# Kernel tuning notes

Measured on AMD Instinct MI355X. Metric: run time of the kernel, lower is better.

The kernel has to match this reference:

```python
import jax, jax.numpy as jnp
import numpy as np

N_NODES = 50000
N_EDGES = 800000
IN_CH = 128
HID = 48
HEADS = 2
HH = HID * HEADS  # 96
N_GRAPHS = 64
NEG_SLOPE = 0.2


def _gat_layer(x, src, dst, n, W, a_src, a_dst, b, heads, out_ch):
    # x: [N, in]; W: [in, heads*out]; a_src/a_dst: [heads, out]; b: [heads*out]
    h = (x @ W).reshape(n, heads, out_ch)              # [N, H, C]
    es = (h * a_src).sum(-1)                            # [N, H]
    ed = (h * a_dst).sum(-1)                            # [N, H]
    e = jax.nn.leaky_relu(es[src] + ed[dst], NEG_SLOPE)  # [E, H]
    m = jax.ops.segment_max(e, dst, num_segments=n)      # segment softmax (stable)
    p = jnp.exp(e - m[dst])
    denom = jax.ops.segment_sum(p, dst, num_segments=n)
    alpha = p / denom[dst]                               # [E, H]
    out = jax.ops.segment_sum(alpha[:, :, None] * h[src], dst, num_segments=n)
    return out.reshape(n, heads * out_ch) + b


def setup_inputs() -> dict:
    key = jax.random.key(0)
    ks = jax.random.split(key, 20)
    x = jax.random.normal(ks[0], (N_NODES, IN_CH), dtype=jnp.float32)
    edge_index = jax.random.randint(ks[1], (2, N_EDGES), 0, N_NODES, dtype=jnp.int64)
    edge_weight = jax.random.uniform(ks[2], (N_EDGES,), dtype=jnp.float32)
    batch = jnp.sort(jax.random.randint(ks[3], (N_NODES,), 0, N_GRAPHS, dtype=jnp.int64))
    s = 0.1
    params = {
        'W1': jax.random.normal(ks[4], (IN_CH, HH)) * s,
        'as1': jax.random.normal(ks[5], (HEADS, HID)) * s,
        'ad1': jax.random.normal(ks[6], (HEADS, HID)) * s,
        'b1': jnp.zeros((HH,), jnp.float32),
        'W2': jax.random.normal(ks[7], (HH, HH)) * s,
        'as2': jax.random.normal(ks[8], (1, HH)) * s,
        'ad2': jax.random.normal(ks[9], (1, HH)) * s,
        'b2': jnp.zeros((HH,), jnp.float32),
        'W3': jax.random.normal(ks[10], (HH, HH)) * s,
        'as3': jax.random.normal(ks[11], (1, HH)) * s,
        'ad3': jax.random.normal(ks[12], (1, HH)) * s,
        'b3': jnp.zeros((HH,), jnp.float32),
        'W4': jax.random.normal(ks[13], (HH, HH)) * s,
        'as4': jax.random.normal(ks[14], (1, HH)) * s,
        'ad4': jax.random.normal(ks[15], (1, HH)) * s,
        'b4': jnp.zeros((HH,), jnp.float32),
        'Wc': jax.random.normal(ks[16], (HH, 1)) * s,
        'bc': jnp.zeros((1,), jnp.float32),
    }
    return {'x': x, 'edge_index': edge_index, 'edge_weight': edge_weight,
            'batch': batch, **params}


def reference(x, edge_index, edge_weight, batch,
              W1, as1, ad1, b1, W2, as2, ad2, b2,
              W3, as3, ad3, b3, W4, as4, ad4, b4, Wc, bc):
    n = x.shape[0]
    loops = jnp.arange(n, dtype=edge_index.dtype)  # PyG GATConv add_self_loops=True
    src = jnp.concatenate([edge_index[0], loops])
    dst = jnp.concatenate([edge_index[1], loops])
    # edge_weight is ignored by GATConv when edge_dim=None (faithful to PyG)
    h = jax.nn.relu(_gat_layer(x, src, dst, n, W1, as1, ad1, b1, HEADS, HID))
    h = jax.nn.relu(_gat_layer(h, src, dst, n, W2, as2, ad2, b2, 1, HH))
    h = jax.nn.relu(_gat_layer(h, src, dst, n, W3, as3, ad3, b3, 1, HH))
    h = jax.nn.relu(_gat_layer(h, src, dst, n, W4, as4, ad4, b4, 1, HH))
    # global_mean_pool
    sums = jax.ops.segment_sum(h, batch, num_segments=N_GRAPHS)
    cnts = jax.ops.segment_sum(jnp.ones((n, 1), h.dtype), batch, num_segments=N_GRAPHS)
    pooled = sums / jnp.maximum(cnts, 1.0)
    return jax.nn.sigmoid(pooled @ Wc + bc)
```

## Files before the change

kernel.cpp:

```cpp
#include <hip/hip_runtime.h>
#include <hip/hip_bf16.h>

#define NN 50000
#define NE 800000
#define NG 64
#define NBUCK 256
#define BN 196
#define EPB 4096
#define HB 196
#define SMAX 4200

typedef __attribute__((ext_vector_type(8))) short short8;
typedef __attribute__((ext_vector_type(4))) float float4v;
typedef __attribute__((ext_vector_type(2))) float float2v;

__device__ __forceinline__ float bf2f(unsigned short u){
    unsigned v = ((unsigned)u) << 16; float f; __builtin_memcpy(&f, &v, 4); return f;
}
__device__ __forceinline__ unsigned short f2bf(float f){
    unsigned u; __builtin_memcpy(&u, &f, 4);
    u = (u + 0x7fffu + ((u >> 16) & 1u)) >> 16;
    return (unsigned short)u;
}
__device__ __forceinline__ float lrelu(float v){ return v > 0.f ? v : 0.2f * v; }

__device__ __forceinline__ float ldflex(const void* p, long i, int isbf){
    if (isbf) return bf2f(((const unsigned short*)p)[i]);
    return ((const float*)p)[i];
}
__device__ __forceinline__ int ldidx(const int* p, long i, int is64){
    return p[is64 ? (i << 1) : i];
}

__device__ __forceinline__ unsigned int enc_fp8_1(float f){
    unsigned u; __builtin_memcpy(&u, &f, 4);
    unsigned s = (u >> 24) & 0x80u;
    float a = fabsf(f); a = fminf(a, 448.f);
    float x = a * 0x1p-120f;
    unsigned xu; __builtin_memcpy(&xu, &x, 4);
    unsigned r = (xu + 0x7FFFFu + ((xu >> 20) & 1u)) >> 20;
    if (r > 0x7Eu) r = 0x7Eu;
    return s | r;
}
__device__ __forceinline__ unsigned short pk_fp8(float a, float b){
#if __has_builtin(__builtin_amdgcn_cvt_pk_fp8_f32)
    int r = __builtin_amdgcn_cvt_pk_fp8_f32(a, b, 0, false);
    return (unsigned short)(r & 0xFFFF);
#else
    return (unsigned short)(enc_fp8_1(a) | (enc_fp8_1(b) << 8));
#endif
}
__device__ __forceinline__ float dec_fp8_manual(unsigned int byte){
    unsigned bits = ((byte & 0x80u) << 24) | ((byte & 0x7Fu) << 20);
    float f; __builtin_memcpy(&f, &bits, 4);
    return f * 0x1p120f;
}
__device__ __forceinline__ void dec_fp8x4_pk(unsigned int v, float2v& lo, float2v& hi){
#if __has_builtin(__builtin_amdgcn_cvt_pk_f32_fp8)
    lo = __builtin_amdgcn_cvt_pk_f32_fp8((int)v, false);
    hi = __builtin_amdgcn_cvt_pk_f32_fp8((int)v, true);
#else
    lo[0] = dec_fp8_manual(v & 0xFF);
    lo[1] = dec_fp8_manual((v >> 8) & 0xFF);
    hi[0] = dec_fp8_manual((v >> 16) & 0xFF);
    hi[1] = dec_fp8_manual((v >> 24) & 0xFF);
#endif
}

__device__ __forceinline__ float rdlane_f(float v, int l){
    int i; __builtin_memcpy(&i, &v, 4);
    int r = __builtin_amdgcn_readlane(i, l);
    float f; __builtin_memcpy(&f, &r, 4);
    return f;
}

__global__ void detect_kernel(const unsigned short* xu, const unsigned int* eiu,
                              const unsigned int* bu, int* flags){
    if (threadIdx.x != 0 || blockIdx.x != 0) return;
    int hit = 0;
    for (int i = 0; i < 128; i++){
        int ex = (xu[2 * i] >> 7) & 0xFF;
        if (ex >= 100 && ex <= 140) hit++;
    }
    flags[0] = (hit >= 64) ? 1 : 0;
    int z = 0;
    for (int i = 0; i < 128; i++) if (eiu[2 * i + 1] == 0) z++;
    flags[1] = (z >= 120) ? 1 : 0;
    z = 0;
    for (int i = 0; i < 128; i++) if (bu[49745 + 2 * i] == 0) z++;
    flags[2] = (z >= 120) ? 1 : 0;
}

__global__ __launch_bounds__(256) void wtprep_kernel(const void* W0, const void* W1,
                                                     const void* W2, const void* W3,
                                                     unsigned short* wt_all,
                                                     const int* flags){
    int l = blockIdx.x;
    const void* W = (l == 0) ? W0 : (l == 1) ? W1 : (l == 2) ? W2 : W3;
    int K = (l == 0) ? 128 : 96;
    unsigned short* out = wt_all + ((l == 0) ? 0 : (96 * 128 + (l - 1) * 96 * 96));
    int isbf = flags[0];
    int tot = 96 * K;
    for (int i = threadIdx.x; i < tot; i += 256){
        int c = i / K, k = i - c * K;
        out[i] = f2bf(ldflex(W, (long)k * 96 + c, isbf));
    }
}

__global__ __launch_bounds__(256) void xconv_kernel(const void* x, unsigned short* xb,
                                                    const int* flags){
    int isbf = flags[0];
    long i8 = ((long)blockIdx.x * 256 + threadIdx.x) * 8;
    if (i8 >= (long)NN * 128) return;
    unsigned int o[4];
    #pragma unroll
    for (int j = 0; j < 4; j++){
        unsigned short a = f2bf(ldflex(x, i8 + 2 * j, isbf));
        unsigned short b = f2bf(ldflex(x, i8 + 2 * j + 1, isbf));
        o[j] = (unsigned)a | ((unsigned)b << 16);
    }
    *(uint4*)(xb + i8) = make_uint4(o[0], o[1], o[2], o[3]);
}

__global__ __launch_bounds__(256) void bhist_kernel(const int* __restrict__ ei,
                                                    int* __restrict__ bcnt,
                                                    const int* __restrict__ flags){
    __shared__ int h[NBUCK];
    int tid = threadIdx.x;
    h[tid] = 0; __syncthreads();
    int f64 = flags[1];
    long e0 = (long)blockIdx.x * EPB + tid;
    #pragma unroll
    for (int r = 0; r < 16; r++){
        long e = e0 + r * 256;
        if (e < NE){
            int d = ldidx(ei, NE + e, f64);
            atomicAdd(&h[d / BN], 1);
        }
    }
    __syncthreads();
    atomicAdd(&bcnt[tid], h[tid]);
}

__global__ __launch_bounds__(256) void bscan_kernel(const int* __restrict__ bcnt,
                                                    int* __restrict__ bbase,
                                                    int* __restrict__ bcur){
    __shared__ int sd[NBUCK];
    int tid = threadIdx.x;
    int v = bcnt[tid];
    sd[tid] = v; __syncthreads();
    for (int off = 1; off < 256; off <<= 1){
        int x = sd[tid];
        int y = (tid >= off) ? sd[tid - off] : 0;
        __syncthreads();
        sd[tid] = x + y;
        __syncthreads();
    }
    int excl = sd[tid] - v;
    bbase[tid] = excl;
    bcur[tid] = excl;
    if (tid == 255) bbase[256] = excl + v;
}

__global__ __launch_bounds__(256) void bscatter_kernel(const int* __restrict__ ei,
                                                       int* __restrict__ bcur,
                                                       int2* __restrict__ ebuf,
                                                       const int* __restrict__ flags){
    __shared__ int h[NBUCK], lofs[NBUCK], gbase[NBUCK], lcur[NBUCK];
    __shared__ int2 lstage[EPB];
    int tid = threadIdx.x;
    int f64 = flags[1];
    h[tid] = 0; __syncthreads();
    int2 ed[16]; int bk[16];
    long e0 = (long)blockIdx.x * EPB + tid;
    #pragma unroll
    for (int r = 0; r < 16; r++){
        long e = e0 + r * 256;
        if (e < NE){
            int s = ldidx(ei, e, f64);
            int d = ldidx(ei, NE + e, f64);
            ed[r] = make_int2(s, d);
            bk[r] = d / BN;
            atomicAdd(&h[bk[r]], 1);
        } else bk[r] = -1;
    }
    __syncthreads();
    int v = h[tid];
    lofs[tid] = v; __syncthreads();
    for (int off = 1; off < 256; off <<= 1){
        int x = lofs[tid];
        int y = (tid >= off) ? lofs[tid - off] : 0;
        __syncthreads();
        lofs[tid] = x + y;
        __syncthreads();
    }
    int excl = lofs[tid] - v;
    lofs[tid] = excl;
    lcur[tid] = excl;
    if (v > 0) gbase[tid] = atomicAdd(&bcur[tid], v);
    __syncthreads();
    #pragma unroll
    for (int r = 0; r < 16; r++){
        if (bk[r] >= 0){
            int p = atomicAdd(&lcur[bk[r]], 1);
            lstage[p] = ed[r];
        }
    }
    __syncthreads();
    long base = (long)blockIdx.x * EPB;
    int cnt = (NE - base < EPB) ? (int)(NE - base) : EPB;
    for (int j = tid; j < cnt; j += 256){
        int2 e = lstage[j];
        int i = e.y / BN;
        ebuf[gbase[i] + j - lofs[i]] = e;
    }
}

__global__ __launch_bounds__(256) void place_kernel(const int2* __restrict__ ebuf,
                                                    const int* __restrict__ bbase,
                                                    int* __restrict__ row_ptr,
                                                    int2* __restrict__ csr2){
    __shared__ int nh[BN];
    __shared__ int nofs[256];
    __shared__ int lcur[BN];
    __shared__ int2 stage[SMAX];
    int k = blockIdx.x, tid = threadIdx.x;
    int n0 = k * BN;
    int seg0 = bbase[k], len = bbase[k + 1] - seg0;
    for (int i = tid; i < BN; i += 256) nh[i] = 0;
    __syncthreads();
    for (int j = tid; j < len; j += 256){
        int2 e = ebuf[seg0 + j];
        atomicAdd(&nh[e.y - n0], 1);
    }
    __syncthreads();
    int v = (tid < BN) ? nh[tid] : 0;
    nofs[tid] = v; __syncthreads();
    for (int off = 1; off < 256; off <<= 1){
        int x = nofs[tid];
        int y = (tid >= off) ? nofs[tid - off] : 0;
        __syncthreads();
        nofs[tid] = x + y;
        __syncthreads();
    }
    int excl = nofs[tid] - v;
    if (tid < BN){
        lcur[tid] = excl;
        int node = n0 + tid;
        if (node < NN) row_ptr[node] = seg0 + excl;
    }
    if (k == NBUCK - 1 && tid == 0) row_ptr[NN] = NE;
    __syncthreads();
    if (len <= SMAX){
        for (int j = tid; j < len; j += 256){
            int2 e = ebuf[seg0 + j];
            int p = atomicAdd(&lcur[e.y - n0], 1);
            stage[p] = e;
        }
        __syncthreads();
        for (int j = tid; j < len; j += 256)
            csr2[seg0 + j] = stage[j];
    } else {
        for (int j = tid; j < len; j += 256){
            int2 e = ebuf[seg0 + j];
            int p = atomicAdd(&lcur[e.y - n0], 1);
            csr2[seg0 + p] = e;
        }
    }
}

template<int K, int H>
__global__ __launch_bounds__(256) void gemm_mfma(const unsigned short* __restrict__ A,
                                                 const unsigned short* __restrict__ Wt,
                                                 const void* __restrict__ as_,
                                                 const void* __restrict__ ad_,
                                                 unsigned short* __restrict__ hq16,
                                                 float* __restrict__ es,
                                                 float* __restrict__ ed,
                                                 float* __restrict__ pself,
                                                 const int* __restrict__ flags){
    __shared__ union {
        struct { unsigned short xs[64 * 40]; unsigned short wt[96 * 40]; } s;
        float hs[64 * 104];
    } u;
    int tid = threadIdx.x;
    int row0 = blockIdx.x * 64;
    int lane = tid & 63, w = tid >> 6;
    int m = lane & 15, q = lane >> 4;
    float4v acc[6];
    #pragma unroll
    for (int ct = 0; ct < 6; ct++) acc[ct] = (float4v){0.f, 0.f, 0.f, 0.f};

    int sr = tid >> 2, kp = tid & 3;
    int rr = row0 + sr; if (rr >= NN) rr = NN - 1;

    for (int k0 = 0; k0 < K; k0 += 32){
        *(uint4*)(u.s.xs + sr * 40 + kp * 8) =
            *(const uint4*)(A + (size_t)rr * K + k0 + kp * 8);
        for (int i = tid; i < 96 * 4; i += 256){
            int c = i >> 2, kq = i & 3;
            *(uint4*)(u.s.wt + c * 40 + kq * 8) =
                *(const uint4*)(Wt + (size_t)c * K + k0 + kq * 8);
        }
        __syncthreads();
        short8 a = *(const short8*)(u.s.xs + (w * 16 + m) * 40 + q * 8);
        #pragma unroll
        for (int ct = 0; ct < 6; ct++){
            short8 b = *(const short8*)(u.s.wt + (ct * 16 + m) * 40 + q * 8);
            acc[ct] = __builtin_amdgcn_mfma_f32_16x16x32_bf16(a, b, acc[ct], 0, 0, 0);
        }
        __syncthreads();
    }

    #pragma unroll
    for (int ct = 0; ct < 6; ct++)
        #pragma unroll
        for (int r = 0; r < 4; r++)
            u.hs[(w * 16 + q * 4 + r) * 104 + ct * 16 + m] = acc[ct][r];
    __syncthreads();

    int rl = tid >> 2, part = tid & 3;
    int row = row0 + rl;
    int isbf = flags[0];
    float hv[24];
    #pragma unroll
    for (int jj = 0; jj < 6; jj++)
        *(float4v*)&hv[jj * 4] = *(const float4v*)&u.hs[rl * 104 + part * 24 + jj * 4];

    float pes = 0.f, ped = 0.f;
    #pragma unroll
    for (int i = 0; i < 24; i++){
        int c = part * 24 + i;
        pes += hv[i] * ldflex(as_, c, isbf);
        ped += hv[i] * ldflex(ad_, c, isbf);
    }
    pes += __shfl_xor(pes, 1); ped += __shfl_xor(ped, 1);
    if (H == 1){ pes += __shfl_xor(pes, 2); ped += __shfl_xor(ped, 2); }

    if (row < NN){
        if (part == 0){
            es[(long)row * H] = pes; ed[(long)row * H] = ped;
            pself[(long)row * H] = __expf(lrelu(pes + ped));
        }
        if (H == 2 && part == 2){
            es[(long)row * H + 1] = pes; ed[(long)row * H + 1] = ped;
            pself[(long)row * H + 1] = __expf(lrelu(pes + ped));
        }
        unsigned short wds[12];
        #pragma unroll
        for (int j = 0; j < 12; j++) wds[j] = pk_fp8(hv[2 * j], hv[2 * j + 1]);
        uint2* dst = (uint2*)hq16 + (long)row * 16 + part * 3;
        #pragma unroll
        for (int j2 = 0; j2 < 3; j2++){
            uint2 v;
            v.x = (unsigned)wds[4 * j2] | ((unsigned)wds[4 * j2 + 1] << 16);
            v.y = (unsigned)wds[4 * j2 + 2] | ((unsigned)wds[4 * j2 + 3] << 16);
            dst[j2] = v;
        }
    }
}

template<int H>
__global__ __launch_bounds__(256) void pexp_kernel(const float* __restrict__ es,
                                                   const float* __restrict__ ed,
                                                   const int2* __restrict__ csr2,
                                                   void* __restrict__ edata){
    int i = blockIdx.x * 256 + threadIdx.x;
    if (i >= NE) return;
    int2 e = csr2[i];
    if (H == 1){
        float p = __expf(lrelu(es[e.x] + ed[e.y]));
        ((uint2*)edata)[i] = make_uint2((unsigned)e.x, __float_as_uint(p));
    } else {
        float p0 = __expf(lrelu(es[2 * (long)e.x] + ed[2 * (long)e.y]));
        float p1 = __expf(lrelu(es[2 * (long)e.x + 1] + ed[2 * (long)e.y + 1]));
        ((uint4*)edata)[i] = make_uint4((unsigned)e.x, __float_as_uint(p0),
                                        __float_as_uint(p1), 0u);
    }
}

template<int H>
__global__ __launch_bounds__(256) void attn_kernel(const unsigned int* __restrict__ hq,
                                                   const void* __restrict__ edata,
                                                   const float* __restrict__ pself,
                                                   const int* __restrict__ row_ptr,
                                                   const void* __restrict__ bias,
                                                   unsigned int* __restrict__ outb,
                                                   const int* __restrict__ flags){
    int lane = threadIdx.x & 63;
    int d = blockIdx.x * 4 + (threadIdx.x >> 6);
    if (d >= NN) return;
    int isbf = flags[0];
    int beg = row_ptr[d], deg = row_ptr[d + 1] - beg;
    int g = (lane >= 24 && lane < 48) ? 1 : 0;
    int c = lane - g * 24;
    bool head0 = (c < 12);
    int m = lane - 48;

    int s_nxt = 0; float p0_nxt = 0.f, p1_nxt = 0.f;
    if (lane >= 48 && m < deg){
        if (H == 1){
            uint2 e = ((const uint2*)edata)[beg + m];
            s_nxt = (int)e.x; p0_nxt = __uint_as_float(e.y);
        } else {
            uint4 e = ((const uint4*)edata)[beg + m];
            s_nxt = (int)e.x; p0_nxt = __uint_as_float(e.y); p1_nxt = __uint_as_float(e.z);
        }
    }

    float2v acc01 = {0.f, 0.f}, acc23 = {0.f, 0.f};
    float dn0 = 0.f, dn1 = 0.f;
    for (int base = 0; base < deg; base += 16){
        int s_cur = s_nxt; float p0c = p0_nxt, p1c = p1_nxt;
        dn0 += p0c; dn1 += p1c;
        int nb = base + 16;
        s_nxt = 0; p0_nxt = 0.f; p1_nxt = 0.f;
        if (lane >= 48 && nb + m < deg){
            if (H == 1){
                uint2 e = ((const uint2*)edata)[beg + nb + m];
                s_nxt = (int)e.x; p0_nxt = __uint_as_float(e.y);
            } else {
                uint4 e = ((const uint4*)edata)[beg + nb + m];
                s_nxt = (int)e.x; p0_nxt = __uint_as_float(e.y); p1_nxt = __uint_as_float(e.z);
            }
        }
        unsigned int v[8]; float pv[8];
        #pragma unroll
        for (int jj = 0; jj < 8; jj++){
            int idx = 48 + 2 * jj + g;
            int s = __shfl(s_cur, idx);
            float p0 = __shfl(p0c, idx);
            float p;
            if (H == 2){
                float p1 = __shfl(p1c, idx);
                p = head0 ? p0 : p1;
            } else p = p0;
            pv[jj] = p;
            v[jj] = (lane < 48) ? hq[(unsigned)s * 32u + (unsigned)c] : 0u;
        }
        #pragma unroll
        for (int jj = 0; jj < 8; jj++){
            float2v lo, hi;
            dec_fp8x4_pk(v[jj], lo, hi);
            float2v p2 = {pv[jj], pv[jj]};
            acc01 += p2 * lo;
            acc23 += p2 * hi;
        }
    }

    for (int off = 1; off < 16; off <<= 1){
        dn0 += __shfl_xor(dn0, off);
        if (H == 2) dn1 += __shfl_xor(dn1, off);
    }
    float dn0_t = rdlane_f(dn0, 48);
    float dn1_t = (H == 2) ? rdlane_f(dn1, 48) : dn0_t;

    float tot[4] = {acc01[0], acc01[1], acc23[0], acc23[1]};
    #pragma unroll
    for (int k = 0; k < 4; k++) tot[k] += __shfl(tot[k], lane + 24);

    if (lane < 24){
        int head = (H == 2) ? (head0 ? 0 : 1) : 0;
        float ps = pself[(long)d * H + head];
        float dn = (head0 ? dn0_t : dn1_t) + ps;
        if (H == 1) dn = dn0_t + ps;
        float2v lo, hi;
        dec_fp8x4_pk(hq[(unsigned)d * 32u + (unsigned)c], lo, hi);
        float o0 = fmaxf((tot[0] + ps * lo[0]) / dn + ldflex(bias, 4 * c + 0, isbf), 0.f);
        float o1 = fmaxf((tot[1] + ps * lo[1]) / dn + ldflex(bias, 4 * c + 1, isbf), 0.f);
        float o2 = fmaxf((tot[2] + ps * hi[0]) / dn + ldflex(bias, 4 * c + 2, isbf), 0.f);
        float o3 = fmaxf((tot[3] + ps * hi[1]) / dn + ldflex(bias, 4 * c + 3, isbf), 0.f);
        uint2 vv;
        vv.x = (unsigned)f2bf(o0) | ((unsigned)f2bf(o1) << 16);
        vv.y = (unsigned)f2bf(o2) | ((unsigned)f2bf(o3) << 16);
        ((uint2*)outb)[(long)d * 24 + c] = vv;
    }
}

__global__ __launch_bounds__(64) void pool_kernel(const unsigned int* __restrict__ bufb,
                                                  const int* __restrict__ batch,
                                                  float* __restrict__ pooled,
                                                  int* __restrict__ gcnt,
                                                  const int* __restrict__ flags){
    int f64 = flags[2];
    int n0 = blockIdx.x * 32;
    if (n0 >= NN) return;
    int n1 = n0 + 32; if (n1 > NN) n1 = NN;
    int lane = threadIdx.x;
    if (lane < 48){
        float a0 = 0.f, a1 = 0.f;
        int curg = ldidx(batch, n0, f64);
        for (int nd = n0; nd < n1; nd++){
            int g = ldidx(batch, nd, f64);
            if (g != curg){
                atomicAdd(&pooled[curg * 96 + 2 * lane], a0);
                atomicAdd(&pooled[curg * 96 + 2 * lane + 1], a1);
                a0 = a1 = 0.f; curg = g;
            }
            unsigned v = bufb[(long)nd * 48 + lane];
            a0 += bf2f((unsigned short)v);
            a1 += bf2f((unsigned short)(v >> 16));
        }
        atomicAdd(&pooled[curg * 96 + 2 * lane], a0);
        atomicAdd(&pooled[curg * 96 + 2 * lane + 1], a1);
    } else if (lane == 48){
        int cnt = 0;
        int curg = ldidx(batch, n0, f64);
        for (int nd = n0; nd < n1; nd++){
            int g = ldidx(batch, nd, f64);
            if (g != curg){
                atomicAdd(&gcnt[curg], cnt);
                cnt = 0; curg = g;
            }
            cnt++;
        }
        atomicAdd(&gcnt[curg], cnt);
    }
}

__global__ void final_kernel(const float* __restrict__ pooled, const int* __restrict__ gcnt,
                             const void* __restrict__ Wc, const void* __restrict__ bc,
                             void* __restrict__ outp, const int* __restrict__ flags){
    int isbf = flags[0];
    int g = threadIdx.x;
    if (g >= NG) return;
    float cnt = (float)gcnt[g];
    if (cnt < 1.f) cnt = 1.f;
    float acc = 0.f;
    for (int c = 0; c < 96; c++)
        acc += (pooled[g * 96 + c] / cnt) * ldflex(Wc, c, isbf);
    acc += ldflex(bc, 0, isbf);
    float sg = 1.f / (1.f + __expf(-acc));
    if (isbf) ((unsigned short*)outp)[g] = f2bf(sg);
    else      ((float*)outp)[g] = sg;
}

extern "C" void kernel_launch(void* const* d_in, const int* in_sizes, int n_in,
                              void* d_out, int out_size, void* d_ws, size_t ws_size,
                              hipStream_t stream){
    const void* x     = d_in[0];
    const int* ei     = (const int*)d_in[1];
    const int* batch  = (const int*)d_in[3];
    const void* W[4]  = {d_in[4],  d_in[8],  d_in[12], d_in[16]};
    const void* AS[4] = {d_in[5],  d_in[9],  d_in[13], d_in[17]};
    const void* AD[4] = {d_in[6],  d_in[10], d_in[14], d_in[18]};
    const void* B[4]  = {d_in[7],  d_in[11], d_in[15], d_in[19]};
    const void* Wc    = d_in[20];
    const void* bc    = d_in[21];

    char* p = (char*)d_ws;
    auto alloc = [&](size_t bytes) -> void* {
        void* r = (void*)p;
        p += (bytes + 255) & ~(size_t)255;
        return r;
    };
    int* flags     = (int*)alloc(16);
    unsigned int* hq = (unsigned int*)alloc((size_t)NN * 128);
    unsigned int* buf1b = (unsigned int*)alloc((size_t)NN * 96 * 2);
    void* xb_edata = alloc((size_t)NE * 16);
    unsigned short* xb = (unsigned short*)xb_edata;
    void* edata = xb_edata;
    unsigned short* wt_all = (unsigned short*)alloc((size_t)(96 * 128 + 3 * 96 * 96) * 2);
    float* es      = (float*)alloc((size_t)NN * 2 * 4);
    float* ed      = (float*)alloc((size_t)NN * 2 * 4);
    float* pself   = (float*)alloc((size_t)NN * 2 * 4);
    int* row_ptr   = (int*)alloc((size_t)(NN + 1) * 4);
    int2* csr2     = (int2*)alloc((size_t)NE * 8);
    int2* ebuf     = (int2*)alloc((size_t)NE * 8);
    int* bcnt      = (int*)alloc((size_t)NBUCK * 4);
    int* bbase     = (int*)alloc((size_t)(NBUCK + 1) * 4);
    int* bcur      = (int*)alloc((size_t)NBUCK * 4);
    float* pooled  = (float*)alloc((size_t)NG * 96 * 4);
    int* gcnt      = (int*)alloc((size_t)NG * 4);

    detect_kernel<<<1, 64, 0, stream>>>((const unsigned short*)x, (const unsigned int*)ei,
                                        (const unsigned int*)batch, flags);

    wtprep_kernel<<<4, 256, 0, stream>>>(W[0], W[1], W[2], W[3], wt_all, flags);
    xconv_kernel<<<3125, 256, 0, stream>>>(x, xb, flags);

    hipMemsetAsync(bcnt, 0, (size_t)NBUCK * 4, stream);
    bhist_kernel<<<HB, 256, 0, stream>>>(ei, bcnt, flags);
    bscan_kernel<<<1, 256, 0, stream>>>(bcnt, bbase, bcur);
    bscatter_kernel<<<HB, 256, 0, stream>>>(ei, bcur, ebuf, flags);
    place_kernel<<<NBUCK, 256, 0, stream>>>(ebuf, bbase, row_ptr, csr2);

    const int GB = (NN + 63) / 64;
    const int AB = (NN + 3) / 4;
    const int EB = (NE + 255) / 256;
    unsigned short* wt1 = wt_all;
    unsigned short* wt2 = wt_all + 96 * 128;
    unsigned short* wt3 = wt2 + 96 * 96;
    unsigned short* wt4 = wt3 + 96 * 96;

    gemm_mfma<128, 2><<<GB, 256, 0, stream>>>(xb, wt1, AS[0], AD[0],
                                              (unsigned short*)hq, es, ed, pself, flags);
    pexp_kernel<2><<<EB, 256, 0, stream>>>(es, ed, csr2, edata);
    attn_kernel<2><<<AB, 256, 0, stream>>>(hq, edata, pself, row_ptr, B[0], buf1b, flags);
    unsigned short* wts[3] = {wt2, wt3, wt4};
    for (int l = 1; l < 4; l++){
        gemm_mfma<96, 1><<<GB, 256, 0, stream>>>((const unsigned short*)buf1b, wts[l - 1],
                                                 AS[l], AD[l],
                                                 (unsigned short*)hq, es, ed, pself, flags);
        pexp_kernel<1><<<EB, 256, 0, stream>>>(es, ed, csr2, edata);
        attn_kernel<1><<<AB, 256, 0, stream>>>(hq, edata, pself, row_ptr, B[l], buf1b, flags);
    }

    hipMemsetAsync(pooled, 0, (size_t)NG * 96 * 4, stream);
    hipMemsetAsync(gcnt, 0, (size_t)NG * 4, stream);
    pool_kernel<<<(NN + 31) / 32, 64, 0, stream>>>(buf1b, batch, pooled, gcnt, flags);
    final_kernel<<<1, 64, 0, stream>>>(pooled, gcnt, Wc, bc, d_out, flags);
}
```

Before: 433.7 us.

## Fuse input conversion into first GEMM, fold memsets, skip empty edge slots

The separate fp32-to-bf16 conversion kernel is removed, and the first-layer GEMM now converts fp32 input rows on the fly while loading its A tile. The three memsets are folded into an extra block of the detect kernel to cut launch count. The attention kernel gains a partial-chunk path that loops only over valid edges when fewer than 16 remain, skipping wasted gathers for low-degree nodes. This trades a little extra branching and GEMM-side conversion work for fewer launches and less memory traffic.

```diff
diff --git a/kernel.cpp b/kernel.cpp
--- a/kernel.cpp
+++ b/kernel.cpp
@@ -75,8 +75,16 @@
 }
 
 __global__ void detect_kernel(const unsigned short* xu, const unsigned int* eiu,
-                              const unsigned int* bu, int* flags){
-    if (threadIdx.x != 0 || blockIdx.x != 0) return;
+                              const unsigned int* bu, int* flags, int* bcnt,
+                              float* pooled, int* gcnt){
+    if (blockIdx.x == 1){
+        int tid = threadIdx.x;
+        bcnt[tid] = 0;
+        for (int i = tid; i < NG * 96; i += 256) pooled[i] = 0.f;
+        if (tid < NG) gcnt[tid] = 0;
+        return;
+    }
+    if (threadIdx.x != 0) return;
     int hit = 0;
     for (int i = 0; i < 128; i++){
         int ex = (xu[2 * i] >> 7) & 0xFF;
@@ -107,21 +115,6 @@
     }
 }
 
-__global__ __launch_bounds__(256) void xconv_kernel(const void* x, unsigned short* xb,
-                                                    const int* flags){
-    int isbf = flags[0];
-    long i8 = ((long)blockIdx.x * 256 + threadIdx.x) * 8;
-    if (i8 >= (long)NN * 128) return;
-    unsigned int o[4];
-    #pragma unroll
-    for (int j = 0; j < 4; j++){
-        unsigned short a = f2bf(ldflex(x, i8 + 2 * j, isbf));
-        unsigned short b = f2bf(ldflex(x, i8 + 2 * j + 1, isbf));
-        o[j] = (unsigned)a | ((unsigned)b << 16);
-    }
-    *(uint4*)(xb + i8) = make_uint4(o[0], o[1], o[2], o[3]);
-}
-
 __global__ __launch_bounds__(256) void bhist_kernel(const int* __restrict__ ei,
                                                     int* __restrict__ bcnt,
                                                     const int* __restrict__ flags){
@@ -269,8 +262,8 @@
     }
 }
 
-template<int K, int H>
-__global__ __launch_bounds__(256) void gemm_mfma(const unsigned short* __restrict__ A,
+template<int K, int H, bool L1>
+__global__ __launch_bounds__(256) void gemm_mfma(const void* __restrict__ Ain,
                                                  const unsigned short* __restrict__ Wt,
                                                  const void* __restrict__ as_,
                                                  const void* __restrict__ ad_,
@@ -287,6 +280,7 @@
     int row0 = blockIdx.x * 64;
     int lane = tid & 63, w = tid >> 6;
     int m = lane & 15, q = lane >> 4;
+    int isbf = flags[0];
     float4v acc[6];
     #pragma unroll
     for (int ct = 0; ct < 6; ct++) acc[ct] = (float4v){0.f, 0.f, 0.f, 0.f};
@@ -295,8 +289,19 @@
     int rr = row0 + sr; if (rr >= NN) rr = NN - 1;
 
     for (int k0 = 0; k0 < K; k0 += 32){
-        *(uint4*)(u.s.xs + sr * 40 + kp * 8) =
-            *(const uint4*)(A + (size_t)rr * K + k0 + kp * 8);
+        uint4 av;
+        if (L1 && !isbf){
+            const float* xf = (const float*)Ain + (size_t)rr * K + k0 + kp * 8;
+            float4 f1 = *(const float4*)xf;
+            float4 f2 = *(const float4*)(xf + 4);
+            av.x = (unsigned)f2bf(f1.x) | ((unsigned)f2bf(f1.y) << 16);
+            av.y = (unsigned)f2bf(f1.z) | ((unsigned)f2bf(f1.w) << 16);
+            av.z = (unsigned)f2bf(f2.x) | ((unsigned)f2bf(f2.y) << 16);
+            av.w = (unsigned)f2bf(f2.z) | ((unsigned)f2bf(f2.w) << 16);
+        } else {
+            av = *(const uint4*)((const unsigned short*)Ain + (size_t)rr * K + k0 + kp * 8);
+        }
+        *(uint4*)(u.s.xs + sr * 40 + kp * 8) = av;
         for (int i = tid; i < 96 * 4; i += 256){
             int c = i >> 2, kq = i & 3;
             *(uint4*)(u.s.wt + c * 40 + kq * 8) =
@@ -321,7 +326,6 @@
 
     int rl = tid >> 2, part = tid & 3;
     int row = row0 + rl;
-    int isbf = flags[0];
     float hv[24];
     #pragma unroll
     for (int jj = 0; jj < 6; jj++)
@@ -424,27 +428,48 @@
                 s_nxt = (int)e.x; p0_nxt = __uint_as_float(e.y); p1_nxt = __uint_as_float(e.z);
             }
         }
-        unsigned int v[8]; float pv[8];
-        #pragma unroll
-        for (int jj = 0; jj < 8; jj++){
-            int idx = 48 + 2 * jj + g;
-            int s = __shfl(s_cur, idx);
-            float p0 = __shfl(p0c, idx);
-            float p;
-            if (H == 2){
-                float p1 = __shfl(p1c, idx);
-                p = head0 ? p0 : p1;
-            } else p = p0;
-            pv[jj] = p;
-            v[jj] = (lane < 48) ? hq[(unsigned)s * 32u + (unsigned)c] : 0u;
-        }
-        #pragma unroll
-        for (int jj = 0; jj < 8; jj++){
-            float2v lo, hi;
-            dec_fp8x4_pk(v[jj], lo, hi);
-            float2v p2 = {pv[jj], pv[jj]};
-            acc01 += p2 * lo;
-            acc23 += p2 * hi;
+        int cnt = deg - base; if (cnt > 16) cnt = 16;
+        if (cnt == 16){
+            unsigned int v[8]; float pv[8];
+            #pragma unroll
+            for (int jj = 0; jj < 8; jj++){
+                int idx = 48 + 2 * jj + g;
+                int s = __shfl(s_cur, idx);
+                float p0 = __shfl(p0c, idx);
+                float p;
+                if (H == 2){
+                    float p1 = __shfl(p1c, idx);
+                    p = head0 ? p0 : p1;
+                } else p = p0;
+                pv[jj] = p;
+                v[jj] = (lane < 48) ? hq[(unsigned)s * 32u + (unsigned)c] : 0u;
+            }
+            #pragma unroll
+            for (int jj = 0; jj < 8; jj++){
+                float2v lo, hi;
+                dec_fp8x4_pk(v[jj], lo, hi);
+                float2v p2 = {pv[jj], pv[jj]};
+                acc01 += p2 * lo;
+                acc23 += p2 * hi;
+            }
+        } else {
+            int njj = (cnt + 1) >> 1;
+            for (int jj = 0; jj < njj; jj++){
+                int idx = 48 + 2 * jj + g;
+                int s = __shfl(s_cur, idx);
+                float p0 = __shfl(p0c, idx);
+                float p;
+                if (H == 2){
+                    float p1 = __shfl(p1c, idx);
+                    p = head0 ? p0 : p1;
+                } else p = p0;
+                unsigned int v = (lane < 48) ? hq[(unsigned)s * 32u + (unsigned)c] : 0u;
+                float2v lo, hi;
+                dec_fp8x4_pk(v, lo, hi);
+                float2v p2 = {p, p};
+                acc01 += p2 * lo;
+                acc23 += p2 * hi;
+            }
         }
     }
 
@@ -557,9 +582,7 @@
     int* flags     = (int*)alloc(16);
     unsigned int* hq = (unsigned int*)alloc((size_t)NN * 128);
     unsigned int* buf1b = (unsigned int*)alloc((size_t)NN * 96 * 2);
-    void* xb_edata = alloc((size_t)NE * 16);
-    unsigned short* xb = (unsigned short*)xb_edata;
-    void* edata = xb_edata;
+    void* edata    = alloc((size_t)NE * 16);
     unsigned short* wt_all = (unsigned short*)alloc((size_t)(96 * 128 + 3 * 96 * 96) * 2);
     float* es      = (float*)alloc((size_t)NN * 2 * 4);
     float* ed      = (float*)alloc((size_t)NN * 2 * 4);
@@ -573,13 +596,10 @@
     float* pooled  = (float*)alloc((size_t)NG * 96 * 4);
     int* gcnt      = (int*)alloc((size_t)NG * 4);
 
-    detect_kernel<<<1, 64, 0, stream>>>((const unsigned short*)x, (const unsigned int*)ei,
-                                        (const unsigned int*)batch, flags);
-
+    detect_kernel<<<2, 256, 0, stream>>>((const unsigned short*)x, (const unsigned int*)ei,
+                                         (const unsigned int*)batch, flags, bcnt, pooled, gcnt);
     wtprep_kernel<<<4, 256, 0, stream>>>(W[0], W[1], W[2], W[3], wt_all, flags);
-    xconv_kernel<<<3125, 256, 0, stream>>>(x, xb, flags);
-
-    hipMemsetAsync(bcnt, 0, (size_t)NBUCK * 4, stream);
+
     bhist_kernel<<<HB, 256, 0, stream>>>(ei, bcnt, flags);
     bscan_kernel<<<1, 256, 0, stream>>>(bcnt, bbase, bcur);
     bscatter_kernel<<<HB, 256, 0, stream>>>(ei, bcur, ebuf, flags);
@@ -593,21 +613,18 @@
     unsigned short* wt3 = wt2 + 96 * 96;
     unsigned short* wt4 = wt3 + 96 * 96;
 
-    gemm_mfma<128, 2><<<GB, 256, 0, stream>>>(xb, wt1, AS[0], AD[0],
-                                              (unsigned short*)hq, es, ed, pself, flags);
+    gemm_mfma<128, 2, true><<<GB, 256, 0, stream>>>(x, wt1, AS[0], AD[0],
+                                                    (unsigned short*)hq, es, ed, pself, flags);
     pexp_kernel<2><<<EB, 256, 0, stream>>>(es, ed, csr2, edata);
     attn_kernel<2><<<AB, 256, 0, stream>>>(hq, edata, pself, row_ptr, B[0], buf1b, flags);
     unsigned short* wts[3] = {wt2, wt3, wt4};
     for (int l = 1; l < 4; l++){
-        gemm_mfma<96, 1><<<GB, 256, 0, stream>>>((const unsigned short*)buf1b, wts[l - 1],
-                                                 AS[l], AD[l],
-                                                 (unsigned short*)hq, es, ed, pself, flags);
+        gemm_mfma<96, 1, false><<<GB, 256, 0, stream>>>(buf1b, wts[l - 1], AS[l], AD[l],
+                                                        (unsigned short*)hq, es, ed, pself, flags);
         pexp_kernel<1><<<EB, 256, 0, stream>>>(es, ed, csr2, edata);
         attn_kernel<1><<<AB, 256, 0, stream>>>(hq, edata, pself, row_ptr, B[l], buf1b, flags);
     }
 
-    hipMemsetAsync(pooled, 0, (size_t)NG * 96 * 4, stream);
-    hipMemsetAsync(gcnt, 0, (size_t)NG * 4, stream);
     pool_kernel<<<(NN + 31) / 32, 64, 0, stream>>>(buf1b, batch, pooled, gcnt, flags);
     final_kernel<<<1, 64, 0, stream>>>(pooled, gcnt, Wc, bc, d_out, flags);
 }
```

Measured after the change: 421.6 us. 2.8% less time.
